# Kernel optimization log

Hardware: AMD Instinct MI355X
Metric: run time of the kernel (lower is better)

Reference implementation:

```python
import jax, jax.numpy as jnp
import numpy as np

# Module hyperparameters (from init_kwargs)
L = 32        # spatial length
CIN = 128     # in_channels
COUT = 256    # out_channels
N = 8         # num_filters
STRIDE = 1
K = 9         # kernel_size (l//4+1 default for l>16)


def setup_inputs() -> dict:
    key = jax.random.key(0)
    kx, kw = jax.random.split(key)
    x = jax.random.normal(kx, (32, CIN, L, L), dtype=jnp.float32)
    # weight init: uniform in [-r, r], r = sqrt(1/(cin*k*k)), shape (n, cin//8, k, k)
    r = np.sqrt(1.0 / (CIN * K * K)).astype(np.float32)
    weight = (jax.random.uniform(kw, (N, CIN // 8, K, K), dtype=jnp.float32) - 0.5) * 2.0 * r
    return {"x": x, "weight": weight}


def reference(x, weight):
    # 3D real FFT over (channel, H, W) of the input: [B, CIN, L, L//2+1] complex
    x_hat = jnp.fft.rfftn(x, axes=(1, 2, 3))
    # Zero-pad weight (cin//8 -> CIN, k -> L) and transform: [N, CIN, L, L//2+1]
    w_hat = jnp.fft.rfftn(weight, s=(CIN, L, L))
    # Broadcast multiply (no channel reduction): [B, N, CIN, L, L//2+1]
    freq_out = jnp.einsum('bchw,nchw->bnchw', x_hat, w_hat)
    # Inverse 3D real FFT over (channel, H, W): [B, N, CIN, L, L]
    out = jnp.fft.irfftn(freq_out, axes=(2, 3, 4))
    # Channel shrink: keep every shrink_ratio-th channel -> CIN/shrink = COUT/N channels
    shrink_ratio = N * CIN // COUT
    out = out[:, :, ::shrink_ratio]                       # [B, N, COUT//N, L, L]
    out = out.reshape(out.shape[0], -1, out.shape[3], out.shape[4])  # [B, COUT, L, L]
    if STRIDE == 2:
        out = out[:, :, ::2, ::2]
    return out
```

## Files before the change

kernel.cpp:

```cpp
#include <hip/hip_runtime.h>

typedef __attribute__((ext_vector_type(4))) float  f32x4;
typedef __attribute__((ext_vector_type(8))) short  s16x8;

#define KK 9

__device__ inline unsigned short f2bf(float f) {
    union { float f; unsigned int u; } v; v.f = f;
    unsigned int u = v.u + 0x7FFFu + ((v.u >> 16) & 1u);
    return (unsigned short)(u >> 16);
}

__global__ void prep_w(const float* __restrict__ wgt, unsigned short* __restrict__ Bg) {
    int idx = blockIdx.x * 256 + threadIdx.x;
    if (idx >= 41 * 4 * 16 * 8) return;
    int e = idx & 7;
    int n = (idx >> 3) & 15;
    int g = (idx >> 7) & 3;
    int c = idx >> 9;
    int k  = c * 32 + g * 8 + e;
    int p  = k >> 4;
    int cp = k & 15;
    float val = 0.f;
    if (n < 8 && p < 81) {
        int ky = p / 9;
        int kx = p - ky * 9;
        int dc = 15 - cp;
        val = wgt[((n * 16 + dc) * KK + ky) * KK + kx];
    }
    Bg[idx] = f2bf(val);
}

__global__ __launch_bounds__(256) void fconv_mfma(
    const float* __restrict__ x,
    const unsigned short* __restrict__ Bg,
    float* __restrict__ out)
{
    __shared__ unsigned short xs[16384];
    char* smb = (char*)xs;

    const int tid = threadIdx.x;
    const int b   = blockIdx.x >> 5;
    const int j   = blockIdx.x & 31;

    const float* xb = x + ((size_t)b << 17);
    int choff[16];
    #pragma unroll
    for (int i = 0; i < 16; ++i)
        choff[i] = ((4 * j - 15 + i) & 127) << 10;

    #pragma unroll
    for (int i = 0; i < 4; ++i) {
        int cell = i * 256 + tid;
        #pragma unroll
        for (int h = 0; h < 2; ++h) {
            union { unsigned short u16[8]; uint4 v; } pk;
            #pragma unroll
            for (int e = 0; e < 8; ++e)
                pk.u16[e] = f2bf(xb[choff[h * 8 + e] + cell]);
            *(uint4*)(smb + h * 16384 + cell * 16) = pk.v;
        }
    }
    __syncthreads();

    const int lane = tid & 63;
    const int wave = tid >> 6;
    const int r    = lane & 15;
    const int g    = lane >> 4;
    const int half = g & 1;
    const int pi   = g >> 1;
    const int y0   = wave * 8;

    f32x4 acc[8][2];
    #pragma unroll
    for (int dy = 0; dy < 8; ++dy) { acc[dy][0] = (f32x4)0.f; acc[dy][1] = (f32x4)0.f; }

    const char* bptr = (const char*)Bg + ((g * 16 + r) << 4);
    s16x8 bfrag = *(const s16x8*)(bptr);

    #pragma unroll 1
    for (int c = 0; c < 41; ++c) {
        int p  = 2 * c + pi;
        int ky = p / 9;
        int kx = p - ky * 9;
        int wr = (r - kx) & 31;
        int yb = (y0 - ky) & 31;
        int abase = (half << 14) + (wr << 4);

        int cn = (c < 40) ? c + 1 : 40;
        s16x8 bnext = *(const s16x8*)(bptr + (cn << 10));

        #pragma unroll
        for (int dy = 0; dy < 8; ++dy) {
            int yy = (yb + dy) & 31;
            int ra = abase + (yy << 9);
            s16x8 a0 = *(const s16x8*)(smb + ra);
            s16x8 a1 = *(const s16x8*)(smb + (ra ^ 256));
            acc[dy][0] = __builtin_amdgcn_mfma_f32_16x16x32_bf16(a0, bfrag, acc[dy][0], 0, 0, 0);
            acc[dy][1] = __builtin_amdgcn_mfma_f32_16x16x32_bf16(a1, bfrag, acc[dy][1], 0, 0, 0);
        }
        bfrag = bnext;
    }

    if (r < 8) {
        float* ob = out + (((size_t)(b * 256 + r * 32 + j)) << 10) + (g << 2);
        #pragma unroll
        for (int dy = 0; dy < 8; ++dy) {
            #pragma unroll
            for (int h = 0; h < 2; ++h) {
                *(float4*)(ob + (y0 + dy) * 32 + h * 16) = *(float4*)&acc[dy][h];
            }
        }
    }
}

__global__ __launch_bounds__(256, 2) void fconv_fallback(
    const float* __restrict__ x,
    const float* __restrict__ wgt,
    float* __restrict__ out)
{
    __shared__ float sw[16 * KK * KK * 8];
    const int tid = threadIdx.x;
    for (int idx = tid; idx < 8 * 16 * KK * KK; idx += 256) {
        int n  = idx / (16 * KK * KK);
        int rm = idx - n * (16 * KK * KK);
        int dc = rm / (KK * KK);
        int r2 = rm - dc * (KK * KK);
        int ky = r2 / KK;
        int kx = r2 - ky * KK;
        sw[((dc * KK + kx) * KK + ky) * 8 + n] = wgt[idx];
    }
    __syncthreads();

    const int bid = blockIdx.x;
    const int b   = bid >> 6;
    const int j   = (bid >> 1) & 31;
    const int yh  = bid & 1;
    const int xw  = tid & 31;
    const int yg  = tid >> 5;
    const int y_base = yh * 16 + yg * 2;

    int rows[10];
    #pragma unroll
    for (int i = 0; i < 10; ++i)
        rows[i] = ((y_base + 24 + i) & 31) << 5;

    float acc[8][2];
    #pragma unroll
    for (int n = 0; n < 8; ++n) { acc[n][0] = 0.f; acc[n][1] = 0.f; }

    const int c0 = 4 * j;
    #pragma unroll 1
    for (int dc = 0; dc < 16; ++dc) {
        const int c_src = (c0 - dc) & 127;
        const float* bx = x + (((size_t)b * 128 + c_src) << 10);
        #pragma unroll 1
        for (int kx = 0; kx < KK; ++kx) {
            const int x_col = (xw - kx) & 31;
            float win[10];
            #pragma unroll
            for (int i = 0; i < 10; ++i)
                win[i] = bx[rows[i] + x_col];
            const float4* wp = (const float4*)&sw[((dc * KK + kx) * KK) * 8];
            #pragma unroll
            for (int ky = 0; ky < KK; ++ky) {
                float4 wA = wp[2 * ky];
                float4 wB = wp[2 * ky + 1];
                float x0 = win[8 - ky];
                float x1 = win[9 - ky];
                acc[0][0] += x0 * wA.x; acc[0][1] += x1 * wA.x;
                acc[1][0] += x0 * wA.y; acc[1][1] += x1 * wA.y;
                acc[2][0] += x0 * wA.z; acc[2][1] += x1 * wA.z;
                acc[3][0] += x0 * wA.w; acc[3][1] += x1 * wA.w;
                acc[4][0] += x0 * wB.x; acc[4][1] += x1 * wB.x;
                acc[5][0] += x0 * wB.y; acc[5][1] += x1 * wB.y;
                acc[6][0] += x0 * wB.z; acc[6][1] += x1 * wB.z;
                acc[7][0] += x0 * wB.w; acc[7][1] += x1 * wB.w;
            }
        }
    }
    #pragma unroll
    for (int n = 0; n < 8; ++n) {
        float* op = out + ((((size_t)b * 256) + n * 32 + j) << 10) + (y_base << 5) + xw;
        op[0]  = acc[n][0];
        op[32] = acc[n][1];
    }
}

extern "C" void kernel_launch(void* const* d_in, const int* in_sizes, int n_in,
                              void* d_out, int out_size, void* d_ws, size_t ws_size,
                              hipStream_t stream) {
    const float* x   = (const float*)d_in[0];
    const float* w   = (const float*)d_in[1];
    float*       out = (float*)d_out;

    const size_t BG_BYTES = 41 * 4 * 16 * 8 * sizeof(unsigned short);
    if (ws_size >= BG_BYTES) {
        unsigned short* Bg = (unsigned short*)d_ws;
        prep_w<<<82, 256, 0, stream>>>(w, Bg);
        fconv_mfma<<<1024, 256, 0, stream>>>(x, Bg, out);
    } else {
        fconv_fallback<<<2048, 256, 0, stream>>>(x, w, out);
    }
}
```

Measured before the change: 114.7 us.

## Pack two kernel rows per MFMA column block and combine via shuffle

The weight matrix now places taps for rows ky and ky+1 into the otherwise-unused columns 8-15 of the MFMA B fragment. This cuts the tap loop from 41 to 23 chunks. After accumulation, the second-row partial sums are shifted by one output row through a lane shuffle, and an LDS handoff carries them across wave boundaries before the results are added and stored. It removes wasted MFMA columns and cuts loop iterations in exchange for extra shuffles, a block-wide barrier and some additional shared memory.

```diff
diff --git a/kernel.cpp b/kernel.cpp
--- a/kernel.cpp
+++ b/kernel.cpp
@@ -4,6 +4,7 @@
 typedef __attribute__((ext_vector_type(8))) short  s16x8;
 
 #define KK 9
+#define NCHUNK 23
 
 __device__ inline unsigned short f2bf(float f) {
     union { float f; unsigned int u; } v; v.f = f;
@@ -13,20 +14,25 @@
 
 __global__ void prep_w(const float* __restrict__ wgt, unsigned short* __restrict__ Bg) {
     int idx = blockIdx.x * 256 + threadIdx.x;
-    if (idx >= 41 * 4 * 16 * 8) return;
-    int e = idx & 7;
-    int n = (idx >> 3) & 15;
-    int g = (idx >> 7) & 3;
-    int c = idx >> 9;
-    int k  = c * 32 + g * 8 + e;
-    int p  = k >> 4;
-    int cp = k & 15;
+    if (idx >= NCHUNK * 4 * 16 * 8) return;
+    int e   = idx & 7;
+    int col = (idx >> 3) & 15;
+    int g   = (idx >> 7) & 3;
+    int c   = idx >> 9;
+    int pi   = g >> 1;
+    int half = g & 1;
+    int cp = half * 8 + e;
+    int dc = 15 - cp;
+    int q  = 2 * c + pi;
+    int n  = col & 7;
+    int t  = col >> 3;
     float val = 0.f;
-    if (n < 8 && p < 81) {
-        int ky = p / 9;
-        int kx = p - ky * 9;
-        int dc = 15 - cp;
-        val = wgt[((n * 16 + dc) * KK + ky) * KK + kx];
+    if (q <= 44) {
+        int ky2 = q / 9;
+        int kx  = q - 9 * ky2;
+        int ky  = 2 * ky2 + t;
+        if (ky <= 8)
+            val = wgt[((n * 16 + dc) * KK + ky) * KK + kx];
     }
     Bg[idx] = f2bf(val);
 }
@@ -36,8 +42,9 @@
     const unsigned short* __restrict__ Bg,
     float* __restrict__ out)
 {
-    __shared__ unsigned short xs[16384];
-    char* smb = (char*)xs;
+    __shared__ char smem[32768 + 4096];
+    char*  smb     = smem;
+    float* handoff = (float*)(smem + 32768);
 
     const int tid = threadIdx.x;
     const int b   = blockIdx.x >> 5;
@@ -79,15 +86,15 @@
     s16x8 bfrag = *(const s16x8*)(bptr);
 
     #pragma unroll 1
-    for (int c = 0; c < 41; ++c) {
-        int p  = 2 * c + pi;
-        int ky = p / 9;
-        int kx = p - ky * 9;
-        int wr = (r - kx) & 31;
-        int yb = (y0 - ky) & 31;
+    for (int c = 0; c < NCHUNK; ++c) {
+        int q   = 2 * c + pi;
+        int ky2 = q / 9;
+        int kx  = q - 9 * ky2;
+        int wr  = (r - kx) & 31;
+        int yb  = (y0 - 2 * ky2) & 31;
         int abase = (half << 14) + (wr << 4);
 
-        int cn = (c < 40) ? c + 1 : 40;
+        int cn = (c < NCHUNK - 1) ? c + 1 : NCHUNK - 1;
         s16x8 bnext = *(const s16x8*)(bptr + (cn << 10));
 
         #pragma unroll
@@ -102,13 +109,37 @@
         bfrag = bnext;
     }
 
+    float recv[8][2][4];
+    #pragma unroll
+    for (int dy = 0; dy < 8; ++dy)
+        #pragma unroll
+        for (int h = 0; h < 2; ++h)
+            #pragma unroll
+            for (int i = 0; i < 4; ++i)
+                recv[dy][h][i] = __shfl_xor(acc[dy][h][i], 8);
+
     if (r < 8) {
+        #pragma unroll
+        for (int h = 0; h < 2; ++h)
+            *(f32x4*)&handoff[wave * 256 + r * 32 + h * 16 + g * 4] = *(f32x4*)recv[7][h];
+    }
+    __syncthreads();
+
+    if (r < 8) {
+        const int pw = (wave + 3) & 3;
+        f32x4 prev[2];
+        #pragma unroll
+        for (int h = 0; h < 2; ++h)
+            prev[h] = *(f32x4*)&handoff[pw * 256 + r * 32 + h * 16 + g * 4];
+
         float* ob = out + (((size_t)(b * 256 + r * 32 + j)) << 10) + (g << 2);
         #pragma unroll
         for (int dy = 0; dy < 8; ++dy) {
             #pragma unroll
             for (int h = 0; h < 2; ++h) {
-                *(float4*)(ob + (y0 + dy) * 32 + h * 16) = *(float4*)&acc[dy][h];
+                f32x4 t1 = (dy == 0) ? prev[h] : *(f32x4*)recv[dy - 1][h];
+                f32x4 v  = acc[dy][h] + t1;
+                *(f32x4*)(ob + (y0 + dy) * 32 + h * 16) = v;
             }
         }
     }
@@ -194,10 +225,10 @@
     const float* w   = (const float*)d_in[1];
     float*       out = (float*)d_out;
 
-    const size_t BG_BYTES = 41 * 4 * 16 * 8 * sizeof(unsigned short);
+    const size_t BG_BYTES = NCHUNK * 4 * 16 * 8 * sizeof(unsigned short);
     if (ws_size >= BG_BYTES) {
         unsigned short* Bg = (unsigned short*)d_ws;
-        prep_w<<<82, 256, 0, stream>>>(w, Bg);
+        prep_w<<<46, 256, 0, stream>>>(w, Bg);
         fconv_mfma<<<1024, 256, 0, stream>>>(x, Bg, out);
     } else {
         fconv_fallback<<<2048, 256, 0, stream>>>(x, w, out);
```

New measurement: 113.3 us. Within noise of the previous version (-1.2%).
